# Kernel tuning notes

Hardware: AMD Instinct MI355X
Metric: run time of the kernel (lower is better)

Reference implementation:

```python
import jax, jax.numpy as jnp
import numpy as np

B, Q, K = 4, 256, 1024
Q_SIZE, K_SIZE, V_SIZE, H = 256, 256, 256, 128
NEG = -1000000.0


def setup_inputs() -> dict:
    key = jax.random.key(0)
    ks = jax.random.split(key, 7)
    return {
        "queries": jax.random.normal(ks[0], (B, Q, Q_SIZE), dtype=jnp.float32),
        "keys": jax.random.normal(ks[1], (B, K, K_SIZE), dtype=jnp.float32),
        "values": jax.random.normal(ks[2], (B, K, V_SIZE), dtype=jnp.float32),
        "valid_lens": jax.random.randint(ks[3], (B,), 1, K + 1),
        # Linear weights stored torch-style: [out_features, in_features]
        "W_q": jax.random.normal(ks[4], (H, Q_SIZE), dtype=jnp.float32) * (1.0 / np.sqrt(Q_SIZE)),
        "W_k": jax.random.normal(ks[5], (H, K_SIZE), dtype=jnp.float32) * (1.0 / np.sqrt(K_SIZE)),
        "w_v": jax.random.normal(ks[6], (H,), dtype=jnp.float32) * (1.0 / np.sqrt(H)),
    }


def reference(queries, keys, values, valid_lens, W_q, W_k, w_v):
    # Projections (torch Linear: x @ W.T)
    q = jnp.einsum("bqi,hi->bqh", queries, W_q)  # [B,Q,H]
    k = jnp.einsum("bki,hi->bkh", keys, W_k)     # [B,K,H]
    # Broadcast add + tanh -> additive scores via dot with w_v
    feat = jnp.tanh(q[:, :, None, :] + k[:, None, :, :])  # [B,Q,K,H]
    scores = jnp.einsum("bqkh,h->bqk", feat, w_v)          # [B,Q,K]
    # masked_softmax: 1-D valid_lens broadcast over all query rows
    mask = jnp.arange(K)[None, None, :] < valid_lens[:, None, None]  # [B,1,K]
    scores = jnp.where(mask, scores, NEG)
    attn = jax.nn.softmax(scores, axis=-1)
    # dropout p=0.0 (eval): identity
    return jnp.einsum("bqk,bkv->bqv", attn, values)  # [B,Q,V]
```

## Files before the change

### kernel.cpp

```cpp
#include <hip/hip_runtime.h>
#include <math.h>

#define BQ   4
#define QN   256
#define KN   1024
#define DIN  256
#define HD   128

#define C2F   2.8853900817779268f
#define NL2E  (-2.8853900817779268f)

__global__ __launch_bounds__(256, 2) void proj_kernel(const float* __restrict__ queries,
                                                      const float* __restrict__ keys,
                                                      const float* __restrict__ W_q,
                                                      const float* __restrict__ W_k,
                                                      float* __restrict__ Eq,
                                                      float* __restrict__ EkT4) {
    __shared__ float xT[32][18];
    __shared__ float WT[32][136];

    const int t = threadIdx.x;
    const int row0 = blockIdx.x * 16;
    const bool is_q = row0 < BQ * QN;
    const float* x = is_q ? queries : keys;
    const float* W = is_q ? W_q : W_k;
    const int xr0 = is_q ? row0 : row0 - BQ * QN;

    const int h0 = (t & 31) * 4;
    const int r0 = (t >> 5) * 2;

    float acc[2][4];
#pragma unroll
    for (int r = 0; r < 2; r++)
#pragma unroll
        for (int c = 0; c < 4; c++) acc[r][c] = 0.f;

    for (int ks = 0; ks < DIN; ks += 32) {
        __syncthreads();
        if (t < 128) {
            const int r = t >> 3, k4 = (t & 7) * 4;
            float4 xv = *(const float4*)(x + (size_t)(xr0 + r) * DIN + ks + k4);
            xT[k4 + 0][r] = xv.x; xT[k4 + 1][r] = xv.y;
            xT[k4 + 2][r] = xv.z; xT[k4 + 3][r] = xv.w;
        }
#pragma unroll
        for (int u = 0; u < 4; u++) {
            const int h = (t >> 3) + 32 * u, k4 = (t & 7) * 4;
            float4 wv = *(const float4*)(W + (size_t)h * DIN + ks + k4);
            WT[k4 + 0][h] = wv.x; WT[k4 + 1][h] = wv.y;
            WT[k4 + 2][h] = wv.z; WT[k4 + 3][h] = wv.w;
        }
        __syncthreads();
#pragma unroll
        for (int kk = 0; kk < 32; kk++) {
            float2 xv = *(const float2*)&xT[kk][r0];
            float4 wv = *(const float4*)&WT[kk][h0];
            const float xr[2] = {xv.x, xv.y};
            const float wc[4] = {wv.x, wv.y, wv.z, wv.w};
#pragma unroll
            for (int r = 0; r < 2; r++)
#pragma unroll
                for (int c = 0; c < 4; c++)
                    acc[r][c] = __builtin_fmaf(xr[r], wc[c], acc[r][c]);
        }
    }

    if (is_q) {
#pragma unroll
        for (int r = 0; r < 2; r++) {
            float4 o;
            o.x = __builtin_amdgcn_exp2f(C2F * acc[r][0]);
            o.y = __builtin_amdgcn_exp2f(C2F * acc[r][1]);
            o.z = __builtin_amdgcn_exp2f(C2F * acc[r][2]);
            o.w = __builtin_amdgcn_exp2f(C2F * acc[r][3]);
            *(float4*)(Eq + (size_t)(row0 + r0 + r) * HD + h0) = o;
        }
    } else {
        const int krow = row0 - BQ * QN;
        const int b = krow >> 10, k0 = (krow & (KN - 1)) + r0;
        const int h4 = t & 31;
#pragma unroll
        for (int r = 0; r < 2; r++) {
            float4 o;
            o.x = __builtin_amdgcn_exp2f(C2F * acc[r][0]);
            o.y = __builtin_amdgcn_exp2f(C2F * acc[r][1]);
            o.z = __builtin_amdgcn_exp2f(C2F * acc[r][2]);
            o.w = __builtin_amdgcn_exp2f(C2F * acc[r][3]);
            *(float4*)(EkT4 + ((size_t)(b * 32 + h4) * KN + k0 + r) * 4) = o;
        }
    }
}

__global__ __launch_bounds__(256, 4) void score_kernel(const float* __restrict__ Eq,
                                                       const float* __restrict__ EkT4,
                                                       const int* __restrict__ valid_lens,
                                                       const float* __restrict__ w_v,
                                                       float* __restrict__ attn,
                                                       float* __restrict__ partial) {
    __shared__ float s_part[2][8][128];
    __shared__ float s_red[4][4];

    const int blk = blockIdx.x;
    const int b = blk & 3;
    const int q0 = ((blk >> 2) & 31) * 8;
    const int c = blk >> 7;
    const int t = threadIdx.x;
    const int valid = valid_lens[b];
    float* pp = partial + (size_t)(b * QN + q0) * 8;

    if (c * 128 >= valid) {
        if (t < 8) pp[t * 8 + c] = 0.f;
        return;
    }

    const int kl = t & 127;
    const int hh = t >> 7;
    const int k = c * 128 + kl;

    const int eqbase = __builtin_amdgcn_readfirstlane((b * QN + q0) * HD + hh * 64);
    const float* eq = Eq + eqbase;
    const float* wp = w_v + __builtin_amdgcn_readfirstlane(hh * 64);

    const float4* kcol = (const float4*)EkT4 + ((size_t)(b * 32 + hh * 16) * KN + k);
    float acc[8] = {0.f, 0.f, 0.f, 0.f, 0.f, 0.f, 0.f, 0.f};

#pragma unroll 4
    for (int i = 0; i < 16; i++) {
        float4 ek4 = kcol[(size_t)i * KN];
        float4 w4 = *(const float4*)(wp + i * 4);
        const float ekv[4] = {ek4.x, ek4.y, ek4.z, ek4.w};
        const float wv4[4] = {w4.x, w4.y, w4.z, w4.w};
#pragma unroll
        for (int q = 0; q < 8; q++) {
            float4 e4 = *(const float4*)(eq + q * HD + i * 4);
            acc[q] = __builtin_fmaf(wv4[0],
                     __builtin_amdgcn_rcpf(__builtin_fmaf(ekv[0], e4.x, 1.0f)), acc[q]);
            acc[q] = __builtin_fmaf(wv4[1],
                     __builtin_amdgcn_rcpf(__builtin_fmaf(ekv[1], e4.y, 1.0f)), acc[q]);
            acc[q] = __builtin_fmaf(wv4[2],
                     __builtin_amdgcn_rcpf(__builtin_fmaf(ekv[2], e4.z, 1.0f)), acc[q]);
            acc[q] = __builtin_fmaf(wv4[3],
                     __builtin_amdgcn_rcpf(__builtin_fmaf(ekv[3], e4.w, 1.0f)), acc[q]);
        }
    }

#pragma unroll
    for (int q = 0; q < 8; q++) s_part[hh][q][kl] = acc[q];
    __syncthreads();

    const int qb = (t >> 7) * 4;
    float* arow = attn + (size_t)(b * QN + q0 + qb) * KN + k;
    float psum[4];
#pragma unroll
    for (int j = 0; j < 4; j++) {
        const int q = qb + j;
        float tot = s_part[0][q][kl] + s_part[1][q][kl];
        float e = (k < valid) ? __builtin_amdgcn_exp2f(NL2E * tot) : 0.f;
        arow[(size_t)j * KN] = e;
#pragma unroll
        for (int off = 32; off > 0; off >>= 1) e += __shfl_xor(e, off, 64);
        psum[j] = e;
    }
    const int wv = t >> 6;
    if ((t & 63) == 0) {
#pragma unroll
        for (int j = 0; j < 4; j++) s_red[wv][j] = psum[j];
    }
    __syncthreads();
    if (t < 8) {
        const int q = t;
        float s = (q < 4) ? (s_red[0][q] + s_red[1][q])
                          : (s_red[2][q - 4] + s_red[3][q - 4]);
        pp[q * 8 + c] = s;
    }
}

__global__ __launch_bounds__(256, 2) void av_kernel(const float* __restrict__ attn,
                                                    const float* __restrict__ partial,
                                                    const float* __restrict__ values,
                                                    const int* __restrict__ valid_lens,
                                                    float* __restrict__ out) {
    __shared__ float s_aT[32][36];
    __shared__ float s_v[32][36];
    __shared__ float s_red[4][32][36];
    __shared__ float s_inv[32];

    const int blk = blockIdx.x;
    const int b = blk & 3;
    const int qt = (blk >> 2) & 7;
    const int vt = blk >> 5;
    const int t = threadIdx.x;
    const int q0 = qt * 32, v0 = vt * 32;
    const int valid = valid_lens[b];
    const int T = (valid + 31) >> 5;

    if (t < 32) {
        const float* pr = partial + (size_t)(b * QN + q0 + t) * 8;
        float4 pA = *(const float4*)pr;
        float4 pB = *(const float4*)(pr + 4);
        s_inv[t] = 1.0f / (pA.x + pA.y + pA.z + pA.w + pB.x + pB.y + pB.z + pB.w);
    }

    const int sr = t >> 3, sc = (t & 7) * 4;
    const float* abase = attn + (size_t)(b * QN + q0 + sr) * KN + sc;
    const float* vbase = values + ((size_t)b * KN + sr) * DIN + v0 + sc;

    const int vh = t & 7, qh = (t >> 3) & 7, ks = t >> 6;

    float acc[4][4];
#pragma unroll
    for (int r = 0; r < 4; r++)
#pragma unroll
        for (int c = 0; c < 4; c++) acc[r][c] = 0.f;

    float4 ra = *(const float4*)abase;
    float4 rv = *(const float4*)vbase;

    for (int tile = 0; tile < T; tile++) {
        __syncthreads();
        s_aT[sc + 0][sr] = ra.x;
        s_aT[sc + 1][sr] = ra.y;
        s_aT[sc + 2][sr] = ra.z;
        s_aT[sc + 3][sr] = ra.w;
        *(float4*)&s_v[sr][sc] = rv;
        __syncthreads();
        if (tile + 1 < T) {
            ra = *(const float4*)(abase + (tile + 1) * 32);
            rv = *(const float4*)(vbase + (size_t)(tile + 1) * 32 * DIN);
        }
#pragma unroll
        for (int i = 0; i < 8; i++) {
            const int kk = ks * 8 + i;
            float4 aq = *(const float4*)&s_aT[kk][qh * 4];
            float4 vv = *(const float4*)&s_v[kk][vh * 4];
            const float ar[4] = {aq.x, aq.y, aq.z, aq.w};
            const float vc[4] = {vv.x, vv.y, vv.z, vv.w};
#pragma unroll
            for (int r = 0; r < 4; r++)
#pragma unroll
                for (int c = 0; c < 4; c++)
                    acc[r][c] = __builtin_fmaf(ar[r], vc[c], acc[r][c]);
        }
    }

#pragma unroll
    for (int r = 0; r < 4; r++)
        *(float4*)&s_red[ks][qh * 4 + r][vh * 4] =
            make_float4(acc[r][0], acc[r][1], acc[r][2], acc[r][3]);
    __syncthreads();

    {
        const int q = t >> 3, v4 = (t & 7) * 4;
        float4 r0 = *(const float4*)&s_red[0][q][v4];
        float4 r1 = *(const float4*)&s_red[1][q][v4];
        float4 r2 = *(const float4*)&s_red[2][q][v4];
        float4 r3 = *(const float4*)&s_red[3][q][v4];
        const float inv = s_inv[q];
        float4 o;
        o.x = (r0.x + r1.x + r2.x + r3.x) * inv;
        o.y = (r0.y + r1.y + r2.y + r3.y) * inv;
        o.z = (r0.z + r1.z + r2.z + r3.z) * inv;
        o.w = (r0.w + r1.w + r2.w + r3.w) * inv;
        *(float4*)(out + (size_t)(b * QN + q0 + q) * DIN + v0 + v4) = o;
    }
}

extern "C" void kernel_launch(void* const* d_in, const int* in_sizes, int n_in,
                              void* d_out, int out_size, void* d_ws, size_t ws_size,
                              hipStream_t stream) {
    const float* queries    = (const float*)d_in[0];
    const float* keys       = (const float*)d_in[1];
    const float* values     = (const float*)d_in[2];
    const int*   valid_lens = (const int*)d_in[3];
    const float* W_q        = (const float*)d_in[4];
    const float* W_k        = (const float*)d_in[5];
    const float* w_v        = (const float*)d_in[6];
    float* out = (float*)d_out;

    float* Eq      = (float*)d_ws;
    float* EkT4    = Eq + (size_t)BQ * QN * HD;
    float* attn    = EkT4 + (size_t)BQ * HD * KN;
    float* partial = attn + (size_t)BQ * QN * KN;

    proj_kernel<<<(BQ * QN + BQ * KN) / 16, 256, 0, stream>>>(queries, keys, W_q, W_k, Eq, EkT4);
    score_kernel<<<BQ * (QN / 8) * 8, 256, 0, stream>>>(Eq, EkT4, valid_lens, w_v, attn, partial);
    av_kernel<<<BQ * 8 * 8, 256, 0, stream>>>(attn, partial, values, valid_lens, out);
}
```

Baseline: 115.9 us.

## Fuse three kernels into one cooperative persistent kernel with grid syncs

Replaces the projection, score and attention-times-values kernels with a single cooperative launch of 256 blocks, separated by grid-wide barriers, so only one launch is paid. The score phase now has each block handle 4 query rows across all keys and normalise the softmax in place, so the partial-sum buffer and the later rescale go away. The price is far less parallelism in the score phase (256 blocks, each looping over all 128 hidden dims and up to 1024 keys) plus the cost of the grid syncs.

```diff
diff --git a/kernel.cpp b/kernel.cpp
--- a/kernel.cpp
+++ b/kernel.cpp
@@ -1,5 +1,8 @@
 #include <hip/hip_runtime.h>
+#include <hip/hip_cooperative_groups.h>
 #include <math.h>
+
+namespace cg = cooperative_groups;
 
 #define BQ   4
 #define QN   256
@@ -10,257 +13,245 @@
 #define C2F   2.8853900817779268f
 #define NL2E  (-2.8853900817779268f)
 
-__global__ __launch_bounds__(256, 2) void proj_kernel(const float* __restrict__ queries,
+union SMem {
+    struct { float xT[32][18]; float WT[32][136]; } p;
+    struct { float red[4][4]; } a;
+    struct { float aT[32][36]; float v[32][36];
+             float red[4][32][36]; } b;
+};
+
+__global__ __launch_bounds__(256, 2) void mono_kernel(const float* __restrict__ queries,
                                                       const float* __restrict__ keys,
+                                                      const float* __restrict__ values,
+                                                      const int* __restrict__ valid_lens,
                                                       const float* __restrict__ W_q,
                                                       const float* __restrict__ W_k,
+                                                      const float* __restrict__ w_v,
                                                       float* __restrict__ Eq,
-                                                      float* __restrict__ EkT4) {
-    __shared__ float xT[32][18];
-    __shared__ float WT[32][136];
-
+                                                      float* __restrict__ EkT4,
+                                                      float* __restrict__ attn,
+                                                      float* __restrict__ out) {
+    cg::grid_group grid = cg::this_grid();
+    __shared__ SMem sm;
+
+    const int bid = blockIdx.x;
     const int t = threadIdx.x;
-    const int row0 = blockIdx.x * 16;
-    const bool is_q = row0 < BQ * QN;
-    const float* x = is_q ? queries : keys;
-    const float* W = is_q ? W_q : W_k;
-    const int xr0 = is_q ? row0 : row0 - BQ * QN;
-
-    const int h0 = (t & 31) * 4;
-    const int r0 = (t >> 5) * 2;
-
-    float acc[2][4];
-#pragma unroll
-    for (int r = 0; r < 2; r++)
-#pragma unroll
-        for (int c = 0; c < 4; c++) acc[r][c] = 0.f;
-
-    for (int ks = 0; ks < DIN; ks += 32) {
-        __syncthreads();
-        if (t < 128) {
-            const int r = t >> 3, k4 = (t & 7) * 4;
-            float4 xv = *(const float4*)(x + (size_t)(xr0 + r) * DIN + ks + k4);
-            xT[k4 + 0][r] = xv.x; xT[k4 + 1][r] = xv.y;
-            xT[k4 + 2][r] = xv.z; xT[k4 + 3][r] = xv.w;
-        }
-#pragma unroll
-        for (int u = 0; u < 4; u++) {
-            const int h = (t >> 3) + 32 * u, k4 = (t & 7) * 4;
-            float4 wv = *(const float4*)(W + (size_t)h * DIN + ks + k4);
-            WT[k4 + 0][h] = wv.x; WT[k4 + 1][h] = wv.y;
-            WT[k4 + 2][h] = wv.z; WT[k4 + 3][h] = wv.w;
-        }
-        __syncthreads();
-#pragma unroll
-        for (int kk = 0; kk < 32; kk++) {
-            float2 xv = *(const float2*)&xT[kk][r0];
-            float4 wv = *(const float4*)&WT[kk][h0];
-            const float xr[2] = {xv.x, xv.y};
-            const float wc[4] = {wv.x, wv.y, wv.z, wv.w};
-#pragma unroll
-            for (int r = 0; r < 2; r++)
-#pragma unroll
-                for (int c = 0; c < 4; c++)
-                    acc[r][c] = __builtin_fmaf(xr[r], wc[c], acc[r][c]);
-        }
+
+    for (int tile = bid; tile < (BQ * QN + BQ * KN) / 16; tile += 256) {
+        const int row0 = tile * 16;
+        const bool is_q = row0 < BQ * QN;
+        const float* x = is_q ? queries : keys;
+        const float* W = is_q ? W_q : W_k;
+        const int xr0 = is_q ? row0 : row0 - BQ * QN;
+
+        const int h0 = (t & 31) * 4;
+        const int r0 = (t >> 5) * 2;
+
+        float acc[2][4];
+#pragma unroll
+        for (int r = 0; r < 2; r++)
+#pragma unroll
+            for (int c = 0; c < 4; c++) acc[r][c] = 0.f;
+
+        for (int ks = 0; ks < DIN; ks += 32) {
+            __syncthreads();
+            if (t < 128) {
+                const int r = t >> 3, k4 = (t & 7) * 4;
+                float4 xv = *(const float4*)(x + (size_t)(xr0 + r) * DIN + ks + k4);
+                sm.p.xT[k4 + 0][r] = xv.x; sm.p.xT[k4 + 1][r] = xv.y;
+                sm.p.xT[k4 + 2][r] = xv.z; sm.p.xT[k4 + 3][r] = xv.w;
+            }
+#pragma unroll
+            for (int u = 0; u < 4; u++) {
+                const int h = (t >> 3) + 32 * u, k4 = (t & 7) * 4;
+                float4 wv = *(const float4*)(W + (size_t)h * DIN + ks + k4);
+                sm.p.WT[k4 + 0][h] = wv.x; sm.p.WT[k4 + 1][h] = wv.y;
+                sm.p.WT[k4 + 2][h] = wv.z; sm.p.WT[k4 + 3][h] = wv.w;
+            }
+            __syncthreads();
+#pragma unroll
+            for (int kk = 0; kk < 32; kk++) {
+                float2 xv = *(const float2*)&sm.p.xT[kk][r0];
+                float4 wv = *(const float4*)&sm.p.WT[kk][h0];
+                const float xr[2] = {xv.x, xv.y};
+                const float wc[4] = {wv.x, wv.y, wv.z, wv.w};
+#pragma unroll
+                for (int r = 0; r < 2; r++)
+#pragma unroll
+                    for (int c = 0; c < 4; c++)
+                        acc[r][c] = __builtin_fmaf(xr[r], wc[c], acc[r][c]);
+            }
+        }
+
+        if (is_q) {
+#pragma unroll
+            for (int r = 0; r < 2; r++) {
+                float4 o;
+                o.x = __builtin_amdgcn_exp2f(C2F * acc[r][0]);
+                o.y = __builtin_amdgcn_exp2f(C2F * acc[r][1]);
+                o.z = __builtin_amdgcn_exp2f(C2F * acc[r][2]);
+                o.w = __builtin_amdgcn_exp2f(C2F * acc[r][3]);
+                *(float4*)(Eq + (size_t)(row0 + r0 + r) * HD + h0) = o;
+            }
+        } else {
+            const int krow = row0 - BQ * QN;
+            const int b = krow >> 10, k0 = (krow & (KN - 1)) + r0;
+            const int h4 = t & 31;
+#pragma unroll
+            for (int r = 0; r < 2; r++) {
+                float4 o;
+                o.x = __builtin_amdgcn_exp2f(C2F * acc[r][0]);
+                o.y = __builtin_amdgcn_exp2f(C2F * acc[r][1]);
+                o.z = __builtin_amdgcn_exp2f(C2F * acc[r][2]);
+                o.w = __builtin_amdgcn_exp2f(C2F * acc[r][3]);
+                *(float4*)(EkT4 + ((size_t)(b * 32 + h4) * KN + k0 + r) * 4) = o;
+            }
+        }
+        __syncthreads();
     }
 
-    if (is_q) {
-#pragma unroll
-        for (int r = 0; r < 2; r++) {
-            float4 o;
-            o.x = __builtin_amdgcn_exp2f(C2F * acc[r][0]);
-            o.y = __builtin_amdgcn_exp2f(C2F * acc[r][1]);
-            o.z = __builtin_amdgcn_exp2f(C2F * acc[r][2]);
-            o.w = __builtin_amdgcn_exp2f(C2F * acc[r][3]);
-            *(float4*)(Eq + (size_t)(row0 + r0 + r) * HD + h0) = o;
-        }
-    } else {
-        const int krow = row0 - BQ * QN;
-        const int b = krow >> 10, k0 = (krow & (KN - 1)) + r0;
-        const int h4 = t & 31;
-#pragma unroll
-        for (int r = 0; r < 2; r++) {
-            float4 o;
-            o.x = __builtin_amdgcn_exp2f(C2F * acc[r][0]);
-            o.y = __builtin_amdgcn_exp2f(C2F * acc[r][1]);
-            o.z = __builtin_amdgcn_exp2f(C2F * acc[r][2]);
-            o.w = __builtin_amdgcn_exp2f(C2F * acc[r][3]);
-            *(float4*)(EkT4 + ((size_t)(b * 32 + h4) * KN + k0 + r) * 4) = o;
-        }
+    __threadfence();
+    grid.sync();
+
+    {
+        const int b = bid & 3;
+        const int q0 = (bid >> 2) * 4;
+        const int valid = valid_lens[b];
+        const int row = b * QN + q0;
+
+        float ev[4][4];
+        float rs[4] = {0.f, 0.f, 0.f, 0.f};
+        const float4* ekbase = (const float4*)EkT4 + (size_t)(b * 32) * KN;
+
+#pragma unroll
+        for (int s = 0; s < 4; s++) {
+            const int k = s * 256 + t;
+            if (s * 256 < valid) {
+                float a[4] = {0.f, 0.f, 0.f, 0.f};
+                const float4* kcol = ekbase + k;
+#pragma unroll 4
+                for (int i = 0; i < 32; i++) {
+                    float4 ek4 = kcol[(size_t)i * KN];
+                    float4 w4 = *(const float4*)(w_v + i * 4);
+                    const float ekv[4] = {ek4.x, ek4.y, ek4.z, ek4.w};
+                    const float wv4[4] = {w4.x, w4.y, w4.z, w4.w};
+#pragma unroll
+                    for (int q = 0; q < 4; q++) {
+                        float4 e4 = *(const float4*)(Eq + (size_t)(row + q) * HD + i * 4);
+                        a[q] = __builtin_fmaf(wv4[0],
+                               __builtin_amdgcn_rcpf(__builtin_fmaf(ekv[0], e4.x, 1.0f)), a[q]);
+                        a[q] = __builtin_fmaf(wv4[1],
+                               __builtin_amdgcn_rcpf(__builtin_fmaf(ekv[1], e4.y, 1.0f)), a[q]);
+                        a[q] = __builtin_fmaf(wv4[2],
+                               __builtin_amdgcn_rcpf(__builtin_fmaf(ekv[2], e4.z, 1.0f)), a[q]);
+                        a[q] = __builtin_fmaf(wv4[3],
+                               __builtin_amdgcn_rcpf(__builtin_fmaf(ekv[3], e4.w, 1.0f)), a[q]);
+                    }
+                }
+#pragma unroll
+                for (int q = 0; q < 4; q++) {
+                    ev[s][q] = (k < valid) ? __builtin_amdgcn_exp2f(NL2E * a[q]) : 0.f;
+                    rs[q] += ev[s][q];
+                }
+            } else {
+#pragma unroll
+                for (int q = 0; q < 4; q++) ev[s][q] = 0.f;
+            }
+        }
+
+#pragma unroll
+        for (int off = 32; off > 0; off >>= 1)
+#pragma unroll
+            for (int q = 0; q < 4; q++) rs[q] += __shfl_xor(rs[q], off, 64);
+        const int wv_ = t >> 6;
+        __syncthreads();
+        if ((t & 63) == 0) {
+#pragma unroll
+            for (int q = 0; q < 4; q++) sm.a.red[wv_][q] = rs[q];
+        }
+        __syncthreads();
+        float inv[4];
+#pragma unroll
+        for (int q = 0; q < 4; q++)
+            inv[q] = 1.0f / (sm.a.red[0][q] + sm.a.red[1][q] + sm.a.red[2][q] + sm.a.red[3][q]);
+
+#pragma unroll
+        for (int s = 0; s < 4; s++)
+#pragma unroll
+            for (int q = 0; q < 4; q++)
+                attn[(size_t)(row + q) * KN + s * 256 + t] = ev[s][q] * inv[q];
     }
-}
-
-__global__ __launch_bounds__(256, 4) void score_kernel(const float* __restrict__ Eq,
-                                                       const float* __restrict__ EkT4,
-                                                       const int* __restrict__ valid_lens,
-                                                       const float* __restrict__ w_v,
-                                                       float* __restrict__ attn,
-                                                       float* __restrict__ partial) {
-    __shared__ float s_part[2][8][128];
-    __shared__ float s_red[4][4];
-
-    const int blk = blockIdx.x;
-    const int b = blk & 3;
-    const int q0 = ((blk >> 2) & 31) * 8;
-    const int c = blk >> 7;
-    const int t = threadIdx.x;
-    const int valid = valid_lens[b];
-    float* pp = partial + (size_t)(b * QN + q0) * 8;
-
-    if (c * 128 >= valid) {
-        if (t < 8) pp[t * 8 + c] = 0.f;
-        return;
-    }
-
-    const int kl = t & 127;
-    const int hh = t >> 7;
-    const int k = c * 128 + kl;
-
-    const int eqbase = __builtin_amdgcn_readfirstlane((b * QN + q0) * HD + hh * 64);
-    const float* eq = Eq + eqbase;
-    const float* wp = w_v + __builtin_amdgcn_readfirstlane(hh * 64);
-
-    const float4* kcol = (const float4*)EkT4 + ((size_t)(b * 32 + hh * 16) * KN + k);
-    float acc[8] = {0.f, 0.f, 0.f, 0.f, 0.f, 0.f, 0.f, 0.f};
-
-#pragma unroll 4
-    for (int i = 0; i < 16; i++) {
-        float4 ek4 = kcol[(size_t)i * KN];
-        float4 w4 = *(const float4*)(wp + i * 4);
-        const float ekv[4] = {ek4.x, ek4.y, ek4.z, ek4.w};
-        const float wv4[4] = {w4.x, w4.y, w4.z, w4.w};
-#pragma unroll
-        for (int q = 0; q < 8; q++) {
-            float4 e4 = *(const float4*)(eq + q * HD + i * 4);
-            acc[q] = __builtin_fmaf(wv4[0],
-                     __builtin_amdgcn_rcpf(__builtin_fmaf(ekv[0], e4.x, 1.0f)), acc[q]);
-            acc[q] = __builtin_fmaf(wv4[1],
-                     __builtin_amdgcn_rcpf(__builtin_fmaf(ekv[1], e4.y, 1.0f)), acc[q]);
-            acc[q] = __builtin_fmaf(wv4[2],
-                     __builtin_amdgcn_rcpf(__builtin_fmaf(ekv[2], e4.z, 1.0f)), acc[q]);
-            acc[q] = __builtin_fmaf(wv4[3],
-                     __builtin_amdgcn_rcpf(__builtin_fmaf(ekv[3], e4.w, 1.0f)), acc[q]);
-        }
-    }
-
-#pragma unroll
-    for (int q = 0; q < 8; q++) s_part[hh][q][kl] = acc[q];
-    __syncthreads();
-
-    const int qb = (t >> 7) * 4;
-    float* arow = attn + (size_t)(b * QN + q0 + qb) * KN + k;
-    float psum[4];
-#pragma unroll
-    for (int j = 0; j < 4; j++) {
-        const int q = qb + j;
-        float tot = s_part[0][q][kl] + s_part[1][q][kl];
-        float e = (k < valid) ? __builtin_amdgcn_exp2f(NL2E * tot) : 0.f;
-        arow[(size_t)j * KN] = e;
-#pragma unroll
-        for (int off = 32; off > 0; off >>= 1) e += __shfl_xor(e, off, 64);
-        psum[j] = e;
-    }
-    const int wv = t >> 6;
-    if ((t & 63) == 0) {
-#pragma unroll
-        for (int j = 0; j < 4; j++) s_red[wv][j] = psum[j];
-    }
-    __syncthreads();
-    if (t < 8) {
-        const int q = t;
-        float s = (q < 4) ? (s_red[0][q] + s_red[1][q])
-                          : (s_red[2][q - 4] + s_red[3][q - 4]);
-        pp[q * 8 + c] = s;
-    }
-}
-
-__global__ __launch_bounds__(256, 2) void av_kernel(const float* __restrict__ attn,
-                                                    const float* __restrict__ partial,
-                                                    const float* __restrict__ values,
-                                                    const int* __restrict__ valid_lens,
-                                                    float* __restrict__ out) {
-    __shared__ float s_aT[32][36];
-    __shared__ float s_v[32][36];
-    __shared__ float s_red[4][32][36];
-    __shared__ float s_inv[32];
-
-    const int blk = blockIdx.x;
-    const int b = blk & 3;
-    const int qt = (blk >> 2) & 7;
-    const int vt = blk >> 5;
-    const int t = threadIdx.x;
-    const int q0 = qt * 32, v0 = vt * 32;
-    const int valid = valid_lens[b];
-    const int T = (valid + 31) >> 5;
-
-    if (t < 32) {
-        const float* pr = partial + (size_t)(b * QN + q0 + t) * 8;
-        float4 pA = *(const float4*)pr;
-        float4 pB = *(const float4*)(pr + 4);
-        s_inv[t] = 1.0f / (pA.x + pA.y + pA.z + pA.w + pB.x + pB.y + pB.z + pB.w);
-    }
-
-    const int sr = t >> 3, sc = (t & 7) * 4;
-    const float* abase = attn + (size_t)(b * QN + q0 + sr) * KN + sc;
-    const float* vbase = values + ((size_t)b * KN + sr) * DIN + v0 + sc;
-
-    const int vh = t & 7, qh = (t >> 3) & 7, ks = t >> 6;
-
-    float acc[4][4];
-#pragma unroll
-    for (int r = 0; r < 4; r++)
-#pragma unroll
-        for (int c = 0; c < 4; c++) acc[r][c] = 0.f;
-
-    float4 ra = *(const float4*)abase;
-    float4 rv = *(const float4*)vbase;
-
-    for (int tile = 0; tile < T; tile++) {
-        __syncthreads();
-        s_aT[sc + 0][sr] = ra.x;
-        s_aT[sc + 1][sr] = ra.y;
-        s_aT[sc + 2][sr] = ra.z;
-        s_aT[sc + 3][sr] = ra.w;
-        *(float4*)&s_v[sr][sc] = rv;
-        __syncthreads();
-        if (tile + 1 < T) {
-            ra = *(const float4*)(abase + (tile + 1) * 32);
-            rv = *(const float4*)(vbase + (size_t)(tile + 1) * 32 * DIN);
-        }
-#pragma unroll
-        for (int i = 0; i < 8; i++) {
-            const int kk = ks * 8 + i;
-            float4 aq = *(const float4*)&s_aT[kk][qh * 4];
-            float4 vv = *(const float4*)&s_v[kk][vh * 4];
-            const float ar[4] = {aq.x, aq.y, aq.z, aq.w};
-            const float vc[4] = {vv.x, vv.y, vv.z, vv.w};
-#pragma unroll
-            for (int r = 0; r < 4; r++)
-#pragma unroll
-                for (int c = 0; c < 4; c++)
-                    acc[r][c] = __builtin_fmaf(ar[r], vc[c], acc[r][c]);
-        }
-    }
-
-#pragma unroll
-    for (int r = 0; r < 4; r++)
-        *(float4*)&s_red[ks][qh * 4 + r][vh * 4] =
-            make_float4(acc[r][0], acc[r][1], acc[r][2], acc[r][3]);
-    __syncthreads();
+
+    __threadfence();
+    grid.sync();
 
     {
+        const int b = bid & 3;
+        const int qt = (bid >> 2) & 7;
+        const int vt = bid >> 5;
+        const int q0 = qt * 32, v0 = vt * 32;
+        const int valid = valid_lens[b];
+        const int T = (valid + 31) >> 5;
+
+        const int sr = t >> 3, sc = (t & 7) * 4;
+        const float* abase = attn + (size_t)(b * QN + q0 + sr) * KN + sc;
+        const float* vbase = values + ((size_t)b * KN + sr) * DIN + v0 + sc;
+
+        const int vh = t & 7, qh = (t >> 3) & 7, ks = t >> 6;
+
+        float acc[4][4];
+#pragma unroll
+        for (int r = 0; r < 4; r++)
+#pragma unroll
+            for (int c = 0; c < 4; c++) acc[r][c] = 0.f;
+
+        float4 ra = *(const float4*)abase;
+        float4 rv = *(const float4*)vbase;
+
+        for (int tile = 0; tile < T; tile++) {
+            __syncthreads();
+            sm.b.aT[sc + 0][sr] = ra.x;
+            sm.b.aT[sc + 1][sr] = ra.y;
+            sm.b.aT[sc + 2][sr] = ra.z;
+            sm.b.aT[sc + 3][sr] = ra.w;
+            *(float4*)&sm.b.v[sr][sc] = rv;
+            __syncthreads();
+            if (tile + 1 < T) {
+                ra = *(const float4*)(abase + (tile + 1) * 32);
+                rv = *(const float4*)(vbase + (size_t)(tile + 1) * 32 * DIN);
+            }
+#pragma unroll
+            for (int i = 0; i < 8; i++) {
+                const int kk = ks * 8 + i;
+                float4 aq = *(const float4*)&sm.b.aT[kk][qh * 4];
+                float4 vv = *(const float4*)&sm.b.v[kk][vh * 4];
+                const float ar[4] = {aq.x, aq.y, aq.z, aq.w};
+                const float vc[4] = {vv.x, vv.y, vv.z, vv.w};
+#pragma unroll
+                for (int r = 0; r < 4; r++)
+#pragma unroll
+                    for (int c = 0; c < 4; c++)
+                        acc[r][c] = __builtin_fmaf(ar[r], vc[c], acc[r][c]);
+            }
+        }
+
+        __syncthreads();
+#pragma unroll
+        for (int r = 0; r < 4; r++)
+            *(float4*)&sm.b.red[ks][qh * 4 + r][vh * 4] =
+                make_float4(acc[r][0], acc[r][1], acc[r][2], acc[r][3]);
+        __syncthreads();
+
         const int q = t >> 3, v4 = (t & 7) * 4;
-        float4 r0 = *(const float4*)&s_red[0][q][v4];
-        float4 r1 = *(const float4*)&s_red[1][q][v4];
-        float4 r2 = *(const float4*)&s_red[2][q][v4];
-        float4 r3 = *(const float4*)&s_red[3][q][v4];
-        const float inv = s_inv[q];
+        float4 r0 = *(const float4*)&sm.b.red[0][q][v4];
+        float4 r1 = *(const float4*)&sm.b.red[1][q][v4];
+        float4 r2 = *(const float4*)&sm.b.red[2][q][v4];
+        float4 r3 = *(const float4*)&sm.b.red[3][q][v4];
         float4 o;
-        o.x = (r0.x + r1.x + r2.x + r3.x) * inv;
-        o.y = (r0.y + r1.y + r2.y + r3.y) * inv;
-        o.z = (r0.z + r1.z + r2.z + r3.z) * inv;
-        o.w = (r0.w + r1.w + r2.w + r3.w) * inv;
+        o.x = r0.x + r1.x + r2.x + r3.x;
+        o.y = r0.y + r1.y + r2.y + r3.y;
+        o.z = r0.z + r1.z + r2.z + r3.z;
+        o.w = r0.w + r1.w + r2.w + r3.w;
         *(float4*)(out + (size_t)(b * QN + q0 + q) * DIN + v0 + v4) = o;
     }
 }
@@ -277,12 +268,13 @@
     const float* w_v        = (const float*)d_in[6];
     float* out = (float*)d_out;
 
-    float* Eq      = (float*)d_ws;
-    float* EkT4    = Eq + (size_t)BQ * QN * HD;
-    float* attn    = EkT4 + (size_t)BQ * HD * KN;
-    float* partial = attn + (size_t)BQ * QN * KN;
-
-    proj_kernel<<<(BQ * QN + BQ * KN) / 16, 256, 0, stream>>>(queries, keys, W_q, W_k, Eq, EkT4);
-    score_kernel<<<BQ * (QN / 8) * 8, 256, 0, stream>>>(Eq, EkT4, valid_lens, w_v, attn, partial);
-    av_kernel<<<BQ * 8 * 8, 256, 0, stream>>>(attn, partial, values, valid_lens, out);
+    float* Eq   = (float*)d_ws;
+    float* EkT4 = Eq + (size_t)BQ * QN * HD;
+    float* attn = EkT4 + (size_t)BQ * HD * KN;
+
+    void* args[] = {(void*)&queries, (void*)&keys, (void*)&values, (void*)&valid_lens,
+                    (void*)&W_q, (void*)&W_k, (void*)&w_v,
+                    (void*)&Eq, (void*)&EkT4, (void*)&attn, (void*)&out};
+    hipLaunchCooperativeKernel((const void*)mono_kernel, dim3(256), dim3(256),
+                               args, 0, stream);
 }
```

After: 245.5 us. +111.8%, slower.
